# Kernel optimization log

Hardware: AMD Instinct MI355X
Metric: run time of the kernel (lower is better)

Reference implementation:

```python
import jax, jax.numpy as jnp
import numpy as np

N_HEADS, N_LEVELS, N_POINTS = 8, 4, 4
D_MODEL, UNIT = 384, 128

@jax.custom_vjp
def grl(x):
    # Gradient Reversal Layer: identity forward, -grad backward (lambda_=1)
    return x

def _grl_fwd(x):
    return x, None

def _grl_bwd(res, g):
    return (-g,)

grl.defvjp(_grl_fwd, _grl_bwd)


def ms_deform_attn_core(value, spatial_shapes_np, loc, attn):
    """Multi-scale deformable attention (grid_sample bilinear, zeros padding, align_corners=False).
    value: (N, Len_in, nH, hd)   loc: (N, Lq, nH, nL, nP, 2) normalized [0,1]   attn: (N, Lq, nH, nL, nP)
    """
    N, Lq, nH, nL, nP, _ = loc.shape
    hd = value.shape[-1]
    b = jnp.arange(N).reshape(N, 1, 1, 1)
    h = jnp.arange(nH).reshape(1, 1, nH, 1)
    out = jnp.zeros((N, Lq, nH, hd), dtype=value.dtype)
    start = 0
    for l in range(nL):
        H, W = int(spatial_shapes_np[l, 0]), int(spatial_shapes_np[l, 1])
        v = value[:, start:start + H * W]  # (N, H*W, nH, hd)
        start += H * W
        # align_corners=False pixel coords
        x = loc[:, :, :, l, :, 0] * W - 0.5
        y = loc[:, :, :, l, :, 1] * H - 0.5
        x0f, y0f = jnp.floor(x), jnp.floor(y)
        lx, ly = x - x0f, y - y0f
        x0, y0 = x0f.astype(jnp.int32), y0f.astype(jnp.int32)
        def gather(xi, yi):
            valid = ((xi >= 0) & (xi < W) & (yi >= 0) & (yi < H)).astype(value.dtype)
            flat = jnp.clip(yi, 0, H - 1) * W + jnp.clip(xi, 0, W - 1)  # (N,Lq,nH,nP)
            return v[b, flat, h] * valid[..., None]  # (N,Lq,nH,nP,hd)
        s = (((1 - lx) * (1 - ly))[..., None] * gather(x0, y0)
             + (lx * (1 - ly))[..., None] * gather(x0 + 1, y0)
             + ((1 - lx) * ly)[..., None] * gather(x0, y0 + 1)
             + (lx * ly)[..., None] * gather(x0 + 1, y0 + 1))
        out = out + jnp.sum(s * attn[:, :, :, l, :, None], axis=3)
    return out.reshape(N, Lq, nH * hd)


def setup_inputs() -> dict:
    key = jax.random.key(0)
    ks = jax.random.split(key, 12)
    N, Lq = 2, 5440
    spatial = np.array([[64, 64], [32, 32], [16, 16], [8, 8]], dtype=np.int32)
    sizes = spatial[:, 0] * spatial[:, 1]
    Len_in = int(sizes.sum())  # 5440
    lsi = np.concatenate([[0], np.cumsum(sizes)[:-1]]).astype(np.int32)
    D, U, nH, nL, nP = D_MODEL, UNIT, N_HEADS, N_LEVELS, N_POINTS
    def lin(k, fin, fout):
        return jax.random.normal(k, (fin, fout), jnp.float32) / np.sqrt(fin)
    # faithful grid-init bias for sampling offsets
    thetas = np.arange(nH) * (2.0 * np.pi / nH)
    grid = np.stack([np.cos(thetas), np.sin(thetas)], -1)
    grid = grid / np.abs(grid).max(-1, keepdims=True)
    grid = np.tile(grid.reshape(nH, 1, 1, 2), (1, nL, nP, 1))
    for i in range(nP):
        grid[:, :, i, :] *= (i + 1)
    return {
        "query": jax.random.normal(ks[0], (N, Lq, D), jnp.float32),
        "reference_points": jax.random.uniform(ks[1], (N, Lq, nL, 2), jnp.float32),
        "input_flatten": jax.random.normal(ks[2], (N, Len_in, D), jnp.float32),
        "input_spatial_shapes": jnp.asarray(spatial),
        "input_level_start_index": jnp.asarray(lsi),
        "W_off": 0.01 * jax.random.normal(ks[3], (2 * U, nH * nL * nP * 2), jnp.float32),
        "b_off": jnp.asarray(grid.reshape(-1), dtype=jnp.float32),
        "W_attn": lin(ks[4], 2 * U, nH * nL * nP),
        "b_attn": jnp.zeros((nH * nL * nP,), jnp.float32),
        "W_val": lin(ks[5], 2 * U, 3 * U),
        "b_val": jnp.zeros((3 * U,), jnp.float32),
        "W_out": lin(ks[6], 3 * U, 2 * U),
        "b_out": jnp.zeros((2 * U,), jnp.float32),
        "W_attn_zd": lin(ks[7], 3 * U, nH * nL * nP),
        "b_attn_zd": jnp.zeros((nH * nL * nP,), jnp.float32),
        "W_val_zd": lin(ks[8], D, D),
        "b_val_zd": jnp.zeros((D,), jnp.float32),
        "W_out_zd": lin(ks[9], D, U),
        "b_out_zd": jnp.zeros((U,), jnp.float32),
    }


def reference(query, reference_points, input_flatten, input_spatial_shapes, input_level_start_index,
              W_off, b_off, W_attn, b_attn, W_val, b_val, W_out, b_out,
              W_attn_zd, b_attn_zd, W_val_zd, b_val_zd, W_out_zd, b_out_zd):
    N, Lq, _ = query.shape
    nH, nL, nP, U = N_HEADS, N_LEVELS, N_POINTS, UNIT
    ss = np.asarray(input_spatial_shapes)  # static level shapes
    sample_query = query[..., :2 * U]
    off = (sample_query @ W_off + b_off).reshape(N, Lq, nH, nL, nP, 2)
    # offset normalizer = [W_l, H_l] per level
    norm = jnp.asarray(np.stack([ss[:, 1], ss[:, 0]], -1), dtype=query.dtype)
    loc = reference_points[:, :, None, :, None, :] + off / norm[None, None, None, :, None, :]
    # top (content) path
    top_val = (input_flatten[..., :2 * U] @ W_val + b_val).reshape(N, -1, nH, 3 * U // nH)
    aw = jax.nn.softmax((sample_query @ W_attn + b_attn).reshape(N, Lq, nH, nL * nP), -1)
    aw = aw.reshape(N, Lq, nH, nL, nP)
    top_out = ms_deform_attn_core(top_val, ss, loc, aw) @ W_out + b_out
    # bottom (domain) path with gradient reversal on content slice
    bot_val_in = jnp.concatenate([grl(input_flatten[..., :2 * U]), input_flatten[..., 2 * U:]], -1)
    bot_val = (bot_val_in @ W_val_zd + b_val_zd).reshape(N, -1, nH, D_MODEL // nH)
    bot_query = jnp.concatenate([grl(query[..., :2 * U]), query[..., 2 * U:]], -1)
    aw_zd = jax.nn.softmax((bot_query @ W_attn_zd + b_attn_zd).reshape(N, Lq, nH, nL * nP), -1)
    aw_zd = aw_zd.reshape(N, Lq, nH, nL, nP)
    bot_out = ms_deform_attn_core(bot_val, ss, loc, aw_zd) @ W_out_zd + b_out_zd
    return jnp.concatenate([top_out, bot_out], -1)
```

## Files before the change

kernel.cpp:

```cpp
#include <hip/hip_runtime.h>
#include <hip/hip_bf16.h>
#include <math.h>

#define DM   384
#define U2   256
#define HD   48

typedef __attribute__((ext_vector_type(8))) short short8;
typedef __attribute__((ext_vector_type(4))) float floatx4;

static __device__ __forceinline__ unsigned short f2bfbits(float f) {
    __hip_bfloat16 h = __float2bfloat16(f);
    return *reinterpret_cast<unsigned short*>(&h);
}
static __device__ __forceinline__ unsigned pack2(float x, float y) {
    return (unsigned)f2bfbits(x) | ((unsigned)f2bfbits(y) << 16);
}
static __device__ __forceinline__ float bflo(unsigned u) { return __uint_as_float(u << 16); }
static __device__ __forceinline__ float bfhi(unsigned u) { return __uint_as_float(u & 0xffff0000u); }

struct PrepParams {
    const float* q; const float* f;
    __hip_bfloat16 *q_bf, *f_bf;
    const float* wsrc[7]; __hip_bfloat16* wdst[7];
    int K[7], N[7], off[8];
    int nQ4, nF4, total;
};
__global__ __launch_bounds__(256) void prep_kernel(PrepParams d) {
    const int idx = blockIdx.x * 256 + threadIdx.x;
    if (idx >= d.total) return;
    if (idx < d.nQ4) {
        const int i4 = idx * 4;
        const float4 v = *(const float4*)&d.q[i4];
        uint2 pk; pk.x = pack2(v.x, v.y); pk.y = pack2(v.z, v.w);
        *(uint2*)&d.q_bf[i4] = pk;
        return;
    }
    if (idx < d.nQ4 + d.nF4) {
        const int i4 = (idx - d.nQ4) * 4;
        const float4 v = *(const float4*)&d.f[i4];
        uint2 pk; pk.x = pack2(v.x, v.y); pk.y = pack2(v.z, v.w);
        *(uint2*)&d.f_bf[i4] = pk;
        return;
    }
    const int iw = idx - d.nQ4 - d.nF4;
    int s = 0;
#pragma unroll
    for (int i = 1; i < 7; ++i) if (iw >= d.off[i]) s = i;
    const int r = iw - d.off[s];
    const int k = r / d.N[s], n = r - k * d.N[s];
    d.wdst[s][(size_t)n * d.K[s] + k] = __float2bfloat16(d.wsrc[s][r]);
}

struct Seg {
    const __hip_bfloat16* A; int lda;
    const __hip_bfloat16* Bt; int ldbt;
    const float* bias; void* C; int ldc; int K; int omode;
};
struct SegParams { Seg seg[5]; int ystart[5]; int nseg; };

__global__ __launch_bounds__(256) void gemm_seg_kernel(SegParams p) {
    __shared__ __hip_bfloat16 Ah[128 * 40];
    __shared__ __hip_bfloat16 Bh[128 * 40];

    const int yb = blockIdx.y;
    int s = 0;
#pragma unroll
    for (int i = 1; i < 5; ++i) if (i < p.nseg && yb >= p.ystart[i]) s = i;
    Seg sg;
    switch (s) {
        case 0: sg = p.seg[0]; break;
        case 1: sg = p.seg[1]; break;
        case 2: sg = p.seg[2]; break;
        case 3: sg = p.seg[3]; break;
        default: sg = p.seg[4]; break;
    }
    const int by = yb - p.ystart[s];

    const int t    = threadIdx.x;
    const int bm   = blockIdx.x * 128;
    const int bn   = by * 128;
    const int w    = t >> 6, lane = t & 63;
    const int wm   = (w >> 1) * 64, wn = (w & 1) * 64;
    const int quad = lane >> 4, lm = lane & 15;

    const int r0 = t >> 2, kc = (t & 3) * 8;

    const __hip_bfloat16* Aptr0 = sg.A  + (size_t)(bm + r0) * sg.lda  + kc;
    const __hip_bfloat16* Aptr1 = sg.A  + (size_t)(bm + r0 + 64) * sg.lda  + kc;
    const __hip_bfloat16* Bptr0 = sg.Bt + (size_t)(bn + r0) * sg.ldbt + kc;
    const __hip_bfloat16* Bptr1 = sg.Bt + (size_t)(bn + r0 + 64) * sg.ldbt + kc;

    short8 aR0 = *(const short8*)Aptr0;
    short8 aR1 = *(const short8*)Aptr1;
    short8 bR0 = *(const short8*)Bptr0;
    short8 bR1 = *(const short8*)Bptr1;

    floatx4 acc[4][4] = {};

    for (int k0 = 0; k0 < sg.K; k0 += 32) {
        *(short8*)&Ah[r0 * 40 + kc]        = aR0;
        *(short8*)&Ah[(r0 + 64) * 40 + kc] = aR1;
        *(short8*)&Bh[r0 * 40 + kc]        = bR0;
        *(short8*)&Bh[(r0 + 64) * 40 + kc] = bR1;
        __syncthreads();

        const int kn = k0 + 32;
        if (kn < sg.K) {
            aR0 = *(const short8*)(Aptr0 + kn);
            aR1 = *(const short8*)(Aptr1 + kn);
            bR0 = *(const short8*)(Bptr0 + kn);
            bR1 = *(const short8*)(Bptr1 + kn);
        }

        short8 af[4], bf[4];
#pragma unroll
        for (int i = 0; i < 4; ++i)
            af[i] = *(const short8*)&Ah[(wm + i * 16 + lm) * 40 + quad * 8];
#pragma unroll
        for (int j = 0; j < 4; ++j)
            bf[j] = *(const short8*)&Bh[(wn + j * 16 + lm) * 40 + quad * 8];
#pragma unroll
        for (int i = 0; i < 4; ++i)
#pragma unroll
            for (int j = 0; j < 4; ++j)
                acc[i][j] = __builtin_amdgcn_mfma_f32_16x16x32_bf16(
                    af[i], bf[j], acc[i][j], 0, 0, 0);
        __syncthreads();
    }

#pragma unroll
    for (int i = 0; i < 4; ++i)
#pragma unroll
        for (int reg = 0; reg < 4; ++reg) {
            const int row = bm + wm + i * 16 + quad * 4 + reg;
#pragma unroll
            for (int j = 0; j < 4; ++j) {
                const int col = bn + wn + j * 16 + lm;
                const float v = acc[i][j][reg] + sg.bias[col];
                if (sg.omode == 0) {
                    ((float*)sg.C)[(size_t)row * sg.ldc + col] = v;
                } else if (sg.omode == 1) {
                    ((__hip_bfloat16*)sg.C)[(size_t)row * sg.ldc + col] = __float2bfloat16(v);
                } else {
                    const int h = col / 48;
                    const size_t idx = (size_t)row * 768 + h * 96 +
                                       ((sg.omode == 3) ? 48 : 0) + (col - h * 48);
                    ((__hip_bfloat16*)sg.C)[idx] = __float2bfloat16(v);
                }
            }
        }
}

#define SPP 524

__global__ __launch_bounds__(192) void sampler_kernel(
    const float* __restrict__ off_buf,
    const float* __restrict__ logit_top,
    const float* __restrict__ logit_bot,
    const float* __restrict__ ref_pts,
    const int*   __restrict__ ss,
    const int*   __restrict__ lsi,
    const __hip_bfloat16* __restrict__ vcomb,
    __hip_bfloat16* __restrict__ core_top,
    __hip_bfloat16* __restrict__ core_bot,
    int Lq, int LenIn)
{
    __shared__ float    sA[4][128];
    __shared__ unsigned sP[4][SPP];

    const int bid = blockIdx.x;
    const int Q0  = bid * 2;
    const int t   = threadIdx.x;

    float gw[2][4];
    int   gp[2][4];
#pragma unroll
    for (int slot = 0; slot < 2; ++slot) {
        const bool active = slot ? (t >= 64) : (t < 128);
        if (!active) continue;
        const int qL = slot;
        const int e  = slot ? (t - 64) : t;
        const int gq = Q0 + qL;
        const int n  = gq / Lq;
        const int l  = (e >> 2) & 3;
        const float2 offv = *(const float2*)&off_buf[(size_t)gq * 256 + 2 * e];
        const float rx = ref_pts[(size_t)(gq * 4 + l) * 2 + 0];
        const float ry = ref_pts[(size_t)(gq * 4 + l) * 2 + 1];
        const int H = ss[2 * l], W = ss[2 * l + 1];
        const int start = lsi[l];

        const float x = (rx + offv.x / (float)W) * (float)W - 0.5f;
        const float y = (ry + offv.y / (float)H) * (float)H - 0.5f;
        const float x0f = floorf(x), y0f = floorf(y);
        const float lx = x - x0f, ly = y - y0f;
        const int ix0 = (int)x0f, iy0 = (int)y0f;
        const int ix1 = ix0 + 1,  iy1 = iy0 + 1;

        const float vx0 = (ix0 >= 0 && ix0 < W) ? 1.f : 0.f;
        const float vx1 = (ix1 >= 0 && ix1 < W) ? 1.f : 0.f;
        const float vy0 = (iy0 >= 0 && iy0 < H) ? 1.f : 0.f;
        const float vy1 = (iy1 >= 0 && iy1 < H) ? 1.f : 0.f;
        const int cx0 = min(max(ix0, 0), W - 1);
        const int cx1 = min(max(ix1, 0), W - 1);
        const int cy0 = min(max(iy0, 0), H - 1);
        const int cy1 = min(max(iy1, 0), H - 1);
        const int base = n * LenIn + start;

        gp[slot][0] = base + cy0 * W + cx0;
        gp[slot][1] = base + cy0 * W + cx1;
        gp[slot][2] = base + cy1 * W + cx0;
        gp[slot][3] = base + cy1 * W + cx1;
        gw[slot][0] = (1.f - lx) * (1.f - ly) * vx0 * vy0;
        gw[slot][1] = lx * (1.f - ly) * vx1 * vy0;
        gw[slot][2] = (1.f - lx) * ly * vx0 * vy1;
        gw[slot][3] = lx * ly * vx1 * vy1;
    }

    if (t < 32) {
        const int q  = t >> 4;
        const int br = (t >> 3) & 1;
        const int h  = t & 7;
        const float* L = (br ? logit_bot : logit_top) + (size_t)(Q0 + q) * 128 + h * 16;
        float lg[16];
        *(float4*)&lg[0]  = *(const float4*)&L[0];
        *(float4*)&lg[4]  = *(const float4*)&L[4];
        *(float4*)&lg[8]  = *(const float4*)&L[8];
        *(float4*)&lg[12] = *(const float4*)&L[12];
        float m = -1e30f;
#pragma unroll
        for (int j = 0; j < 16; ++j) m = fmaxf(m, lg[j]);
        float ex[16], sum = 0.f;
#pragma unroll
        for (int j = 0; j < 16; ++j) { ex[j] = expf(lg[j] - m); sum += ex[j]; }
        const float inv = 1.f / sum;
#pragma unroll
        for (int j = 0; j < 16; ++j) sA[q * 2 + br][h * 16 + j] = ex[j] * inv;
    }
    __syncthreads();

#pragma unroll
    for (int slot = 0; slot < 2; ++slot) {
        const bool active = slot ? (t >= 64) : (t < 128);
        if (!active) continue;
        const int e = slot ? (t - 64) : t;
        const int pidx = 4 * e + (e >> 4);
#pragma unroll
        for (int br = 0; br < 2; ++br) {
            const float a = sA[slot * 2 + br][e];
#pragma unroll
            for (int k = 0; k < 4; ++k) {
                sP[slot * 2 + br][pidx + k] =
                    ((unsigned)f2bfbits(gw[slot][k] * a) << 16) | (unsigned)gp[slot][k];
            }
        }
    }
    __syncthreads();

    const int q  = t / 96;
    const int r  = t - q * 96;
    const int g  = r / 6;
    const int m  = r - g * 6;
    const int br = g & 1;
    const int h  = g >> 1;

    const unsigned* P = sP[q * 2 + br];
    const char* vb = (const char*)vcomb + h * 192 + br * 96 + m * 16;

    float a0 = 0.f, a1 = 0.f, a2 = 0.f, a3 = 0.f;
    float a4 = 0.f, a5 = 0.f, a6 = 0.f, a7 = 0.f;
#pragma unroll 4
    for (int lp = 0; lp < 16; ++lp) {
        const int ib = 65 * h + 4 * lp;
#pragma unroll
        for (int k = 0; k < 4; ++k) {
            const unsigned u = P[ib + k];
            const float wv = __uint_as_float(u & 0xffff0000u);
            const unsigned pt = u & 0x3fffu;
            const uint4 v = *(const uint4*)(vb + pt * 1536u);
            a0 = fmaf(wv, bflo(v.x), a0);
            a1 = fmaf(wv, bfhi(v.x), a1);
            a2 = fmaf(wv, bflo(v.y), a2);
            a3 = fmaf(wv, bfhi(v.y), a3);
            a4 = fmaf(wv, bflo(v.z), a4);
            a5 = fmaf(wv, bfhi(v.z), a5);
            a6 = fmaf(wv, bflo(v.w), a6);
            a7 = fmaf(wv, bfhi(v.w), a7);
        }
    }
    uint4 o;
    o.x = pack2(a0, a1); o.y = pack2(a2, a3);
    o.z = pack2(a4, a5); o.w = pack2(a6, a7);
    __hip_bfloat16* dst = br ? core_bot : core_top;
    *(uint4*)&dst[(size_t)(Q0 + q) * DM + h * HD + m * 8] = o;
}

extern "C" void kernel_launch(void* const* d_in, const int* in_sizes, int n_in,
                              void* d_out, int out_size, void* d_ws, size_t ws_size,
                              hipStream_t stream) {
    const float* query   = (const float*)d_in[0];
    const float* refpts  = (const float*)d_in[1];
    const float* flat    = (const float*)d_in[2];
    const int*   ss      = (const int*)d_in[3];
    const int*   lsi     = (const int*)d_in[4];
    const float* W_off   = (const float*)d_in[5];
    const float* b_off   = (const float*)d_in[6];
    const float* W_attn  = (const float*)d_in[7];
    const float* b_attn  = (const float*)d_in[8];
    const float* W_val   = (const float*)d_in[9];
    const float* b_val   = (const float*)d_in[10];
    const float* W_out   = (const float*)d_in[11];
    const float* b_out   = (const float*)d_in[12];
    const float* W_attn_zd = (const float*)d_in[13];
    const float* b_attn_zd = (const float*)d_in[14];
    const float* W_val_zd  = (const float*)d_in[15];
    const float* b_val_zd  = (const float*)d_in[16];
    const float* W_out_zd  = (const float*)d_in[17];
    const float* b_out_zd  = (const float*)d_in[18];

    const int Lq    = in_sizes[0] / (2 * DM);
    const int LenIn = in_sizes[2] / (2 * DM);
    const int M  = 2 * Lq;
    const int Mv = 2 * LenIn;

    float* out = (float*)d_out;

    float* ws      = (float*)d_ws;
    float* off_buf = ws;
    float* lt      = off_buf + (size_t)M * 256;
    float* lb      = lt + (size_t)M * 128;
    __hip_bfloat16* q_bf  = (__hip_bfloat16*)(lb + (size_t)M * 128);
    __hip_bfloat16* f_bf  = q_bf + (size_t)M * 384;
    __hip_bfloat16* vcomb = f_bf + (size_t)Mv * 384;
    __hip_bfloat16* ct    = vcomb + (size_t)Mv * 768;
    __hip_bfloat16* cb    = ct + (size_t)M * 384;
    __hip_bfloat16* wtb   = cb + (size_t)M * 384;

    PrepParams pp;
    pp.q = query; pp.f = flat;
    pp.q_bf = q_bf; pp.f_bf = f_bf;
    const float* srcs[7] = {W_attn, W_attn_zd, W_val, W_val_zd, W_out, W_out_zd, W_off};
    const int Ks[7] = {256, 384, 256, 384, 384, 384, 256};
    const int Ns[7] = {128, 128, 384, 384, 256, 128, 256};
    __hip_bfloat16* dsts[7];
    int off = 0;
    for (int i = 0; i < 7; ++i) {
        pp.wsrc[i] = srcs[i]; pp.K[i] = Ks[i]; pp.N[i] = Ns[i];
        pp.off[i] = off;
        dsts[i] = wtb + off;
        pp.wdst[i] = dsts[i];
        off += Ks[i] * Ns[i];
    }
    pp.off[7] = off;
    pp.nQ4 = M * DM / 4;
    pp.nF4 = Mv * DM / 4;
    pp.total = pp.nQ4 + pp.nF4 + off;

    const dim3 blk(256);
    const int mg = M / 128;

    prep_kernel<<<dim3((pp.total + 255) / 256), blk, 0, stream>>>(pp);

    {
        SegParams p;
        p.seg[0] = { q_bf, DM, dsts[6], 256, b_off,    off_buf, 256, 256, 0 };
        p.seg[1] = { q_bf, DM, dsts[0], 256, b_attn,   lt,      128, 256, 0 };
        p.seg[2] = { q_bf, DM, dsts[1], 384, b_attn_zd,lb,      128, 384, 0 };
        p.seg[3] = { f_bf, DM, dsts[2], 256, b_val,    vcomb,   0,   256, 2 };
        p.seg[4] = { f_bf, DM, dsts[3], 384, b_val_zd, vcomb,   0,   384, 3 };
        p.ystart[0] = 0; p.ystart[1] = 2; p.ystart[2] = 3;
        p.ystart[3] = 4; p.ystart[4] = 7;
        p.nseg = 5;
        gemm_seg_kernel<<<dim3(mg, 10), blk, 0, stream>>>(p);
    }

    sampler_kernel<<<dim3(M / 2), dim3(192), 0, stream>>>(
        off_buf, lt, lb, refpts, ss, lsi, vcomb, ct, cb, Lq, LenIn);

    {
        SegParams p;
        p.seg[0] = { ct, DM, dsts[4], 384, b_out,    out,      DM, 384, 0 };
        p.seg[1] = { cb, DM, dsts[5], 384, b_out_zd, out + U2, DM, 384, 0 };
        p.ystart[0] = 0; p.ystart[1] = 2;
        p.nseg = 2;
        gemm_seg_kernel<<<dim3(mg, 3), blk, 0, stream>>>(p);
    }
}
```

Measured before the change: 247.8 us.

## Load GEMM tiles directly into LDS and widen sampler blocks to four queries

The GEMM kernel drops its register-staged prefetch of A/B tiles and uses global_load_lds to copy 16-byte chunks straight from global memory into shared memory. The shared tiles lose their 40-element row padding so each wave writes a contiguous 32-row slab. Separately, the sampler kernel now handles four queries per block with 384 threads instead of two queries with 192, which halves the number of blocks and doubles the shared staging arrays. The goal is fewer register round-trips and less per-block overhead. In exchange, the GEMM loses its overlap of the next tile's loads with the current MFMA work, and the unpadded LDS layout may add bank conflicts on fragment reads.

```diff
diff --git a/kernel.cpp b/kernel.cpp
--- a/kernel.cpp
+++ b/kernel.cpp
@@ -18,6 +18,10 @@
 }
 static __device__ __forceinline__ float bflo(unsigned u) { return __uint_as_float(u << 16); }
 static __device__ __forceinline__ float bfhi(unsigned u) { return __uint_as_float(u & 0xffff0000u); }
+
+#define GLDS16(g, l)  __builtin_amdgcn_global_load_lds(                        \
+    (const __attribute__((address_space(1))) unsigned int*)(g),                \
+    (__attribute__((address_space(3))) unsigned int*)(l), 16, 0, 0)
 
 struct PrepParams {
     const float* q; const float* f;
@@ -60,8 +64,8 @@
 struct SegParams { Seg seg[5]; int ystart[5]; int nseg; };
 
 __global__ __launch_bounds__(256) void gemm_seg_kernel(SegParams p) {
-    __shared__ __hip_bfloat16 Ah[128 * 40];
-    __shared__ __hip_bfloat16 Bh[128 * 40];
+    __shared__ __hip_bfloat16 As[128 * 32];
+    __shared__ __hip_bfloat16 Bs[128 * 32];
 
     const int yb = blockIdx.y;
     int s = 0;
@@ -84,42 +88,34 @@
     const int wm   = (w >> 1) * 64, wn = (w & 1) * 64;
     const int quad = lane >> 4, lm = lane & 15;
 
-    const int r0 = t >> 2, kc = (t & 3) * 8;
-
-    const __hip_bfloat16* Aptr0 = sg.A  + (size_t)(bm + r0) * sg.lda  + kc;
-    const __hip_bfloat16* Aptr1 = sg.A  + (size_t)(bm + r0 + 64) * sg.lda  + kc;
-    const __hip_bfloat16* Bptr0 = sg.Bt + (size_t)(bn + r0) * sg.ldbt + kc;
-    const __hip_bfloat16* Bptr1 = sg.Bt + (size_t)(bn + r0 + 64) * sg.ldbt + kc;
-
-    short8 aR0 = *(const short8*)Aptr0;
-    short8 aR1 = *(const short8*)Aptr1;
-    short8 bR0 = *(const short8*)Bptr0;
-    short8 bR1 = *(const short8*)Bptr1;
+    const int sr = lane >> 2;
+    const int sc = (lane & 3) * 8;
+
+    const __hip_bfloat16* Ag0 = sg.A  + (size_t)(bm + 32 * w + sr) * sg.lda  + sc;
+    const __hip_bfloat16* Ag1 = sg.A  + (size_t)(bm + 32 * w + 16 + sr) * sg.lda  + sc;
+    const __hip_bfloat16* Bg0 = sg.Bt + (size_t)(bn + 32 * w + sr) * sg.ldbt + sc;
+    const __hip_bfloat16* Bg1 = sg.Bt + (size_t)(bn + 32 * w + 16 + sr) * sg.ldbt + sc;
+    __hip_bfloat16* Al0 = As + (32 * w) * 32;
+    __hip_bfloat16* Al1 = As + (32 * w + 16) * 32;
+    __hip_bfloat16* Bl0 = Bs + (32 * w) * 32;
+    __hip_bfloat16* Bl1 = Bs + (32 * w + 16) * 32;
 
     floatx4 acc[4][4] = {};
 
     for (int k0 = 0; k0 < sg.K; k0 += 32) {
-        *(short8*)&Ah[r0 * 40 + kc]        = aR0;
-        *(short8*)&Ah[(r0 + 64) * 40 + kc] = aR1;
-        *(short8*)&Bh[r0 * 40 + kc]        = bR0;
-        *(short8*)&Bh[(r0 + 64) * 40 + kc] = bR1;
+        GLDS16(Ag0 + k0, Al0);
+        GLDS16(Ag1 + k0, Al1);
+        GLDS16(Bg0 + k0, Bl0);
+        GLDS16(Bg1 + k0, Bl1);
         __syncthreads();
 
-        const int kn = k0 + 32;
-        if (kn < sg.K) {
-            aR0 = *(const short8*)(Aptr0 + kn);
-            aR1 = *(const short8*)(Aptr1 + kn);
-            bR0 = *(const short8*)(Bptr0 + kn);
-            bR1 = *(const short8*)(Bptr1 + kn);
-        }
-
         short8 af[4], bf[4];
 #pragma unroll
         for (int i = 0; i < 4; ++i)
-            af[i] = *(const short8*)&Ah[(wm + i * 16 + lm) * 40 + quad * 8];
+            af[i] = *(const short8*)&As[(wm + i * 16 + lm) * 32 + quad * 8];
 #pragma unroll
         for (int j = 0; j < 4; ++j)
-            bf[j] = *(const short8*)&Bh[(wn + j * 16 + lm) * 40 + quad * 8];
+            bf[j] = *(const short8*)&Bs[(wn + j * 16 + lm) * 32 + quad * 8];
 #pragma unroll
         for (int i = 0; i < 4; ++i)
 #pragma unroll
@@ -154,7 +150,7 @@
 
 #define SPP 524
 
-__global__ __launch_bounds__(192) void sampler_kernel(
+__global__ __launch_bounds__(384) void sampler_kernel(
     const float* __restrict__ off_buf,
     const float* __restrict__ logit_top,
     const float* __restrict__ logit_bot,
@@ -166,22 +162,21 @@
     __hip_bfloat16* __restrict__ core_bot,
     int Lq, int LenIn)
 {
-    __shared__ float    sA[4][128];
-    __shared__ unsigned sP[4][SPP];
+    __shared__ float    sA[8][128];
+    __shared__ unsigned sP[8][SPP];
 
     const int bid = blockIdx.x;
-    const int Q0  = bid * 2;
+    const int Q0  = bid * 4;
     const int t   = threadIdx.x;
 
     float gw[2][4];
     int   gp[2][4];
 #pragma unroll
     for (int slot = 0; slot < 2; ++slot) {
-        const bool active = slot ? (t >= 64) : (t < 128);
-        if (!active) continue;
-        const int qL = slot;
-        const int e  = slot ? (t - 64) : t;
-        const int gq = Q0 + qL;
+        if (slot && t >= 128) continue;
+        const int q = slot ? 3 : (t >> 7);
+        const int e = slot ? t : (t & 127);
+        const int gq = Q0 + q;
         const int n  = gq / Lq;
         const int l  = (e >> 2) & 3;
         const float2 offv = *(const float2*)&off_buf[(size_t)gq * 256 + 2 * e];
@@ -217,7 +212,7 @@
         gw[slot][3] = lx * ly * vx1 * vy1;
     }
 
-    if (t < 32) {
+    if (t < 64) {
         const int q  = t >> 4;
         const int br = (t >> 3) & 1;
         const int h  = t & 7;
@@ -241,16 +236,16 @@
 
 #pragma unroll
     for (int slot = 0; slot < 2; ++slot) {
-        const bool active = slot ? (t >= 64) : (t < 128);
-        if (!active) continue;
-        const int e = slot ? (t - 64) : t;
+        if (slot && t >= 128) continue;
+        const int q = slot ? 3 : (t >> 7);
+        const int e = slot ? t : (t & 127);
         const int pidx = 4 * e + (e >> 4);
 #pragma unroll
         for (int br = 0; br < 2; ++br) {
-            const float a = sA[slot * 2 + br][e];
+            const float a = sA[q * 2 + br][e];
 #pragma unroll
             for (int k = 0; k < 4; ++k) {
-                sP[slot * 2 + br][pidx + k] =
+                sP[q * 2 + br][pidx + k] =
                     ((unsigned)f2bfbits(gw[slot][k] * a) << 16) | (unsigned)gp[slot][k];
             }
         }
@@ -374,7 +369,7 @@
         gemm_seg_kernel<<<dim3(mg, 10), blk, 0, stream>>>(p);
     }
 
-    sampler_kernel<<<dim3(M / 2), dim3(192), 0, stream>>>(
+    sampler_kernel<<<dim3(M / 4), dim3(384), 0, stream>>>(
         off_buf, lt, lb, refpts, ss, lsi, vcomb, ct, cb, Lq, LenIn);
 
     {
```

Result: slower. 253.9 us (+2.4%).

## Fuse fp32-to-bf16 input conversion into GEMM loads and split sampler per query

Applied to the files above, without the earlier changes.

The prep kernel no longer converts query and input_flatten to bf16. The first GEMM now reads fp32 activations directly and packs them to bf16 while staging into shared memory, which removes a full write and re-read of the converted arrays. The register prefetch (software pipelining) in the GEMM main loop is dropped, so global load latency is no longer hidden behind MFMA work. The sampler now handles one query per block instead of two, splitting the 16 level-point steps across two thread halves and reducing the partial sums through shared memory, which adds an extra barrier.

```diff
diff --git a/kernel.cpp b/kernel.cpp
--- a/kernel.cpp
+++ b/kernel.cpp
@@ -20,30 +20,13 @@
 static __device__ __forceinline__ float bfhi(unsigned u) { return __uint_as_float(u & 0xffff0000u); }
 
 struct PrepParams {
-    const float* q; const float* f;
-    __hip_bfloat16 *q_bf, *f_bf;
     const float* wsrc[7]; __hip_bfloat16* wdst[7];
     int K[7], N[7], off[8];
-    int nQ4, nF4, total;
+    int total;
 };
 __global__ __launch_bounds__(256) void prep_kernel(PrepParams d) {
-    const int idx = blockIdx.x * 256 + threadIdx.x;
-    if (idx >= d.total) return;
-    if (idx < d.nQ4) {
-        const int i4 = idx * 4;
-        const float4 v = *(const float4*)&d.q[i4];
-        uint2 pk; pk.x = pack2(v.x, v.y); pk.y = pack2(v.z, v.w);
-        *(uint2*)&d.q_bf[i4] = pk;
-        return;
-    }
-    if (idx < d.nQ4 + d.nF4) {
-        const int i4 = (idx - d.nQ4) * 4;
-        const float4 v = *(const float4*)&d.f[i4];
-        uint2 pk; pk.x = pack2(v.x, v.y); pk.y = pack2(v.z, v.w);
-        *(uint2*)&d.f_bf[i4] = pk;
-        return;
-    }
-    const int iw = idx - d.nQ4 - d.nF4;
+    const int iw = blockIdx.x * 256 + threadIdx.x;
+    if (iw >= d.total) return;
     int s = 0;
 #pragma unroll
     for (int i = 1; i < 7; ++i) if (iw >= d.off[i]) s = i;
@@ -53,15 +36,15 @@
 }
 
 struct Seg {
-    const __hip_bfloat16* A; int lda;
+    const void* A; int lda; int aty;
     const __hip_bfloat16* Bt; int ldbt;
     const float* bias; void* C; int ldc; int K; int omode;
 };
 struct SegParams { Seg seg[5]; int ystart[5]; int nseg; };
 
 __global__ __launch_bounds__(256) void gemm_seg_kernel(SegParams p) {
-    __shared__ __hip_bfloat16 Ah[128 * 40];
-    __shared__ __hip_bfloat16 Bh[128 * 40];
+    __shared__ __hip_bfloat16 As[128 * 40];
+    __shared__ __hip_bfloat16 Bs[128 * 40];
 
     const int yb = blockIdx.y;
     int s = 0;
@@ -86,40 +69,38 @@
 
     const int r0 = t >> 2, kc = (t & 3) * 8;
 
-    const __hip_bfloat16* Aptr0 = sg.A  + (size_t)(bm + r0) * sg.lda  + kc;
-    const __hip_bfloat16* Aptr1 = sg.A  + (size_t)(bm + r0 + 64) * sg.lda  + kc;
-    const __hip_bfloat16* Bptr0 = sg.Bt + (size_t)(bn + r0) * sg.ldbt + kc;
-    const __hip_bfloat16* Bptr1 = sg.Bt + (size_t)(bn + r0 + 64) * sg.ldbt + kc;
-
-    short8 aR0 = *(const short8*)Aptr0;
-    short8 aR1 = *(const short8*)Aptr1;
-    short8 bR0 = *(const short8*)Bptr0;
-    short8 bR1 = *(const short8*)Bptr1;
-
     floatx4 acc[4][4] = {};
 
     for (int k0 = 0; k0 < sg.K; k0 += 32) {
-        *(short8*)&Ah[r0 * 40 + kc]        = aR0;
-        *(short8*)&Ah[(r0 + 64) * 40 + kc] = aR1;
-        *(short8*)&Bh[r0 * 40 + kc]        = bR0;
-        *(short8*)&Bh[(r0 + 64) * 40 + kc] = bR1;
+#pragma unroll
+        for (int g = 0; g < 2; ++g) {
+            const int row = r0 + 64 * g;
+            if (sg.aty) {
+                *(short8*)&As[row * 40 + kc] =
+                    *(const short8*)((const __hip_bfloat16*)sg.A +
+                        (size_t)(bm + row) * sg.lda + k0 + kc);
+            } else {
+                const float* src = (const float*)sg.A +
+                    (size_t)(bm + row) * sg.lda + k0 + kc;
+                const float4 f0 = *(const float4*)(src + 0);
+                const float4 f1 = *(const float4*)(src + 4);
+                uint4 u;
+                u.x = pack2(f0.x, f0.y); u.y = pack2(f0.z, f0.w);
+                u.z = pack2(f1.x, f1.y); u.w = pack2(f1.z, f1.w);
+                *(uint4*)&As[row * 40 + kc] = u;
+            }
+            *(short8*)&Bs[row * 40 + kc] =
+                *(const short8*)&sg.Bt[(size_t)(bn + row) * sg.ldbt + k0 + kc];
+        }
         __syncthreads();
 
-        const int kn = k0 + 32;
-        if (kn < sg.K) {
-            aR0 = *(const short8*)(Aptr0 + kn);
-            aR1 = *(const short8*)(Aptr1 + kn);
-            bR0 = *(const short8*)(Bptr0 + kn);
-            bR1 = *(const short8*)(Bptr1 + kn);
-        }
-
         short8 af[4], bf[4];
 #pragma unroll
         for (int i = 0; i < 4; ++i)
-            af[i] = *(const short8*)&Ah[(wm + i * 16 + lm) * 40 + quad * 8];
+            af[i] = *(const short8*)&As[(wm + i * 16 + lm) * 40 + quad * 8];
 #pragma unroll
         for (int j = 0; j < 4; ++j)
-            bf[j] = *(const short8*)&Bh[(wn + j * 16 + lm) * 40 + quad * 8];
+            bf[j] = *(const short8*)&Bs[(wn + j * 16 + lm) * 40 + quad * 8];
 #pragma unroll
         for (int i = 0; i < 4; ++i)
 #pragma unroll
@@ -166,27 +147,23 @@
     __hip_bfloat16* __restrict__ core_bot,
     int Lq, int LenIn)
 {
-    __shared__ float    sA[4][128];
-    __shared__ unsigned sP[4][SPP];
+    __shared__ float    sA[2][128];
+    __shared__ unsigned sP[2][SPP];
+    __shared__ float4   sRed[96][2];
 
     const int bid = blockIdx.x;
-    const int Q0  = bid * 2;
     const int t   = threadIdx.x;
 
-    float gw[2][4];
-    int   gp[2][4];
-#pragma unroll
-    for (int slot = 0; slot < 2; ++slot) {
-        const bool active = slot ? (t >= 64) : (t < 128);
-        if (!active) continue;
-        const int qL = slot;
-        const int e  = slot ? (t - 64) : t;
-        const int gq = Q0 + qL;
-        const int n  = gq / Lq;
-        const int l  = (e >> 2) & 3;
-        const float2 offv = *(const float2*)&off_buf[(size_t)gq * 256 + 2 * e];
-        const float rx = ref_pts[(size_t)(gq * 4 + l) * 2 + 0];
-        const float ry = ref_pts[(size_t)(gq * 4 + l) * 2 + 1];
+    float gw[4];
+    int   gp[4];
+
+    if (t < 128) {
+        const int e = t;
+        const int n = bid / Lq;
+        const int l = (e >> 2) & 3;
+        const float2 offv = *(const float2*)&off_buf[(size_t)bid * 256 + 2 * e];
+        const float rx = ref_pts[(size_t)(bid * 4 + l) * 2 + 0];
+        const float ry = ref_pts[(size_t)(bid * 4 + l) * 2 + 1];
         const int H = ss[2 * l], W = ss[2 * l + 1];
         const int start = lsi[l];
 
@@ -205,23 +182,23 @@
         const int cx1 = min(max(ix1, 0), W - 1);
         const int cy0 = min(max(iy0, 0), H - 1);
         const int cy1 = min(max(iy1, 0), H - 1);
-        const int base = n * LenIn + start;
-
-        gp[slot][0] = base + cy0 * W + cx0;
-        gp[slot][1] = base + cy0 * W + cx1;
-        gp[slot][2] = base + cy1 * W + cx0;
-        gp[slot][3] = base + cy1 * W + cx1;
-        gw[slot][0] = (1.f - lx) * (1.f - ly) * vx0 * vy0;
-        gw[slot][1] = lx * (1.f - ly) * vx1 * vy0;
-        gw[slot][2] = (1.f - lx) * ly * vx0 * vy1;
-        gw[slot][3] = lx * ly * vx1 * vy1;
-    }
-
-    if (t < 32) {
-        const int q  = t >> 4;
-        const int br = (t >> 3) & 1;
+        const int base = bid / Lq * LenIn + start;
+        (void)n;
+
+        gp[0] = base + cy0 * W + cx0;
+        gp[1] = base + cy0 * W + cx1;
+        gp[2] = base + cy1 * W + cx0;
+        gp[3] = base + cy1 * W + cx1;
+        gw[0] = (1.f - lx) * (1.f - ly) * vx0 * vy0;
+        gw[1] = lx * (1.f - ly) * vx1 * vy0;
+        gw[2] = (1.f - lx) * ly * vx0 * vy1;
+        gw[3] = lx * ly * vx1 * vy1;
+    }
+
+    if (t < 16) {
+        const int br = t >> 3;
         const int h  = t & 7;
-        const float* L = (br ? logit_bot : logit_top) + (size_t)(Q0 + q) * 128 + h * 16;
+        const float* L = (br ? logit_bot : logit_top) + (size_t)bid * 128 + h * 16;
         float lg[16];
         *(float4*)&lg[0]  = *(const float4*)&L[0];
         *(float4*)&lg[4]  = *(const float4*)&L[4];
@@ -235,48 +212,46 @@
         for (int j = 0; j < 16; ++j) { ex[j] = expf(lg[j] - m); sum += ex[j]; }
         const float inv = 1.f / sum;
 #pragma unroll
-        for (int j = 0; j < 16; ++j) sA[q * 2 + br][h * 16 + j] = ex[j] * inv;
+        for (int j = 0; j < 16; ++j) sA[br][h * 16 + j] = ex[j] * inv;
     }
     __syncthreads();
 
-#pragma unroll
-    for (int slot = 0; slot < 2; ++slot) {
-        const bool active = slot ? (t >= 64) : (t < 128);
-        if (!active) continue;
-        const int e = slot ? (t - 64) : t;
+    if (t < 128) {
+        const int e = t;
         const int pidx = 4 * e + (e >> 4);
 #pragma unroll
         for (int br = 0; br < 2; ++br) {
-            const float a = sA[slot * 2 + br][e];
+            const float a = sA[br][e];
 #pragma unroll
             for (int k = 0; k < 4; ++k) {
-                sP[slot * 2 + br][pidx + k] =
-                    ((unsigned)f2bfbits(gw[slot][k] * a) << 16) | (unsigned)gp[slot][k];
+                sP[br][pidx + k] =
+                    ((unsigned)f2bfbits(gw[k] * a) << 16) | (unsigned)gp[k];
             }
         }
     }
     __syncthreads();
 
-    const int q  = t / 96;
-    const int r  = t - q * 96;
-    const int g  = r / 6;
-    const int m  = r - g * 6;
-    const int br = g & 1;
-    const int h  = g >> 1;
-
-    const unsigned* P = sP[q * 2 + br];
+    const int half = t / 96;
+    const int u    = t - half * 96;
+    const int g    = u / 6;
+    const int m    = u - g * 6;
+    const int br   = g & 1;
+    const int h    = g >> 1;
+
+    const unsigned* P = sP[br];
     const char* vb = (const char*)vcomb + h * 192 + br * 96 + m * 16;
 
     float a0 = 0.f, a1 = 0.f, a2 = 0.f, a3 = 0.f;
     float a4 = 0.f, a5 = 0.f, a6 = 0.f, a7 = 0.f;
-#pragma unroll 4
-    for (int lp = 0; lp < 16; ++lp) {
-        const int ib = 65 * h + 4 * lp;
+    const int lp0 = half * 8;
+#pragma unroll
+    for (int lp = 0; lp < 8; ++lp) {
+        const int ib = 65 * h + 4 * (lp0 + lp);
 #pragma unroll
         for (int k = 0; k < 4; ++k) {
-            const unsigned u = P[ib + k];
-            const float wv = __uint_as_float(u & 0xffff0000u);
-            const unsigned pt = u & 0x3fffu;
+            const unsigned uu = P[ib + k];
+            const float wv = __uint_as_float(uu & 0xffff0000u);
+            const unsigned pt = uu & 0x3fffu;
             const uint4 v = *(const uint4*)(vb + pt * 1536u);
             a0 = fmaf(wv, bflo(v.x), a0);
             a1 = fmaf(wv, bfhi(v.x), a1);
@@ -288,11 +263,25 @@
             a7 = fmaf(wv, bfhi(v.w), a7);
         }
     }
-    uint4 o;
-    o.x = pack2(a0, a1); o.y = pack2(a2, a3);
-    o.z = pack2(a4, a5); o.w = pack2(a6, a7);
-    __hip_bfloat16* dst = br ? core_bot : core_top;
-    *(uint4*)&dst[(size_t)(Q0 + q) * DM + h * HD + m * 8] = o;
+
+    if (half) {
+        float4 p0; p0.x = a0; p0.y = a1; p0.z = a2; p0.w = a3;
+        float4 p1; p1.x = a4; p1.y = a5; p1.z = a6; p1.w = a7;
+        sRed[u][0] = p0;
+        sRed[u][1] = p1;
+    }
+    __syncthreads();
+    if (!half) {
+        const float4 p0 = sRed[u][0];
+        const float4 p1 = sRed[u][1];
+        uint4 o;
+        o.x = pack2(a0 + p0.x, a1 + p0.y);
+        o.y = pack2(a2 + p0.z, a3 + p0.w);
+        o.z = pack2(a4 + p1.x, a5 + p1.y);
+        o.w = pack2(a6 + p1.z, a7 + p1.w);
+        __hip_bfloat16* dst = br ? core_bot : core_top;
+        *(uint4*)&dst[(size_t)bid * DM + h * HD + m * 8] = o;
+    }
 }
 
 extern "C" void kernel_launch(void* const* d_in, const int* in_sizes, int n_in,
@@ -329,16 +318,12 @@
     float* off_buf = ws;
     float* lt      = off_buf + (size_t)M * 256;
     float* lb      = lt + (size_t)M * 128;
-    __hip_bfloat16* q_bf  = (__hip_bfloat16*)(lb + (size_t)M * 128);
-    __hip_bfloat16* f_bf  = q_bf + (size_t)M * 384;
-    __hip_bfloat16* vcomb = f_bf + (size_t)Mv * 384;
+    __hip_bfloat16* vcomb = (__hip_bfloat16*)(lb + (size_t)M * 128);
     __hip_bfloat16* ct    = vcomb + (size_t)Mv * 768;
     __hip_bfloat16* cb    = ct + (size_t)M * 384;
     __hip_bfloat16* wtb   = cb + (size_t)M * 384;
 
     PrepParams pp;
-    pp.q = query; pp.f = flat;
-    pp.q_bf = q_bf; pp.f_bf = f_bf;
     const float* srcs[7] = {W_attn, W_attn_zd, W_val, W_val_zd, W_out, W_out_zd, W_off};
     const int Ks[7] = {256, 384, 256, 384, 384, 384, 256};
     const int Ns[7] = {128, 128, 384, 384, 256, 128, 256};
@@ -352,9 +337,7 @@
         off += Ks[i] * Ns[i];
     }
     pp.off[7] = off;
-    pp.nQ4 = M * DM / 4;
-    pp.nF4 = Mv * DM / 4;
-    pp.total = pp.nQ4 + pp.nF4 + off;
+    pp.total = off;
 
     const dim3 blk(256);
     const int mg = M / 128;
@@ -363,24 +346,24 @@
 
     {
         SegParams p;
-        p.seg[0] = { q_bf, DM, dsts[6], 256, b_off,    off_buf, 256, 256, 0 };
-        p.seg[1] = { q_bf, DM, dsts[0], 256, b_attn,   lt,      128, 256, 0 };
-        p.seg[2] = { q_bf, DM, dsts[1], 384, b_attn_zd,lb,      128, 384, 0 };
-        p.seg[3] = { f_bf, DM, dsts[2], 256, b_val,    vcomb,   0,   256, 2 };
-        p.seg[4] = { f_bf, DM, dsts[3], 384, b_val_zd, vcomb,   0,   384, 3 };
+        p.seg[0] = { query, DM, 0, dsts[6], 256, b_off,     off_buf, 256, 256, 0 };
+        p.seg[1] = { query, DM, 0, dsts[0], 256, b_attn,    lt,      128, 256, 0 };
+        p.seg[2] = { query, DM, 0, dsts[1], 384, b_attn_zd, lb,      128, 384, 0 };
+        p.seg[3] = { flat,  DM, 0, dsts[2], 256, b_val,     vcomb,   0,   256, 2 };
+        p.seg[4] = { flat,  DM, 0, dsts[3], 384, b_val_zd,  vcomb,   0,   384, 3 };
         p.ystart[0] = 0; p.ystart[1] = 2; p.ystart[2] = 3;
         p.ystart[3] = 4; p.ystart[4] = 7;
         p.nseg = 5;
         gemm_seg_kernel<<<dim3(mg, 10), blk, 0, stream>>>(p);
     }
 
-    sampler_kernel<<<dim3(M / 2), dim3(192), 0, stream>>>(
+    sampler_kernel<<<dim3(M), dim3(192), 0, stream>>>(
         off_buf, lt, lb, refpts, ss, lsi, vcomb, ct, cb, Lq, LenIn);
 
     {
         SegParams p;
-        p.seg[0] = { ct, DM, dsts[4], 384, b_out,    out,      DM, 384, 0 };
-        p.seg[1] = { cb, DM, dsts[5], 384, b_out_zd, out + U2, DM, 384, 0 };
+        p.seg[0] = { ct, DM, 1, dsts[4], 384, b_out,    out,      DM, 384, 0 };
+        p.seg[1] = { cb, DM, 1, dsts[5], 384, b_out_zd, out + U2, DM, 384, 0 };
         p.ystart[0] = 0; p.ystart[1] = 2;
         p.nseg = 2;
         gemm_seg_kernel<<<dim3(mg, 3), blk, 0, stream>>>(p);
```

Result: slower. 255.9 us (+3.3%).
